# Kernel tuning notes

Measured on AMD Instinct MI355X. Metric: run time of the kernel, lower is better.

The kernel has to match this reference:

```python
import jax, jax.numpy as jnp
import numpy as np

B, D, NCLS = 65536, 784, 10

def sparse_layer(x, idx, w, b):
    # x: [B, D]; idx: [Dout, k] int; w: [Dout, k]; b: [Dout]
    # out[b, n] = sum_j x[b, idx[n, j]] * w[n, j] + b[n]
    g = x[:, idx]                      # [B, Dout, k] gather
    return jnp.einsum('bnk,nk->bn', g, w) + b

def setup_inputs() -> dict:
    key = jax.random.key(0)
    ks = jax.random.split(key, 12)
    def rn(k, shape, scale):
        return jax.random.normal(k, shape, dtype=jnp.float32) * scale
    return {
        'x': rn(ks[0], (B, D), 1.0),
        'idx1': jax.random.randint(ks[1], (D, 2), 0, D, dtype=jnp.int32),
        'w1': rn(ks[2], (D, 2), 0.5),
        'b1': rn(ks[3], (D,), 0.1),
        'idx2': jax.random.randint(ks[4], (D, 4), 0, D, dtype=jnp.int32),
        'w2': rn(ks[5], (D, 4), 0.4),
        'b2': rn(ks[6], (D,), 0.1),
        'idx3': jax.random.randint(ks[7], (D, 8), 0, D, dtype=jnp.int32),
        'w3': rn(ks[8], (D, 8), 0.3),
        'b3': rn(ks[9], (D,), 0.1),
        'fc_w': rn(ks[10], (NCLS, D), 0.05),
        'fc_b': rn(ks[11], (NCLS,), 0.05),
    }

def reference(x, idx1, w1, b1, idx2, w2, b2, idx3, w3, b3, fc_w, fc_b):
    h = jax.nn.gelu(sparse_layer(x, idx1, w1, b1), approximate=False)
    h = jax.nn.gelu(sparse_layer(h, idx2, w2, b2), approximate=False)
    h = jax.nn.gelu(sparse_layer(h, idx3, w3, b3), approximate=False)
    logits = h @ fc_w.T + fc_b          # [B, 10]
    return jax.nn.softmax(logits, axis=-1)
```

## Files before the change

kernel.cpp:

```cpp
#include <hip/hip_runtime.h>

#define D_     784
#define ROWS   8
#define NCLS   10
#define BLOCK  768
#define NB     (65536 / ROWS)
#define PL     (D_ * 4)
#define TAIL   (D_ - BLOCK)

__device__ __forceinline__ float gelu_f(float x) {
    float x2    = x * x;
    float inner = fmaf(0.044715f * x, x2, x);
    float e     = exp2f(2.3022082f * inner);
    float r     = __builtin_amdgcn_rcpf(e + 1.0f);
    return fmaf(-x, r, x);
}

__device__ __forceinline__ float4 gelu4(const float4& a) {
    return make_float4(gelu_f(a.x), gelu_f(a.y), gelu_f(a.z), gelu_f(a.w));
}

__device__ __forceinline__ void fma4(float4& a, const float4& h4, float wk) {
    a.x = fmaf(h4.x, wk, a.x);
    a.y = fmaf(h4.y, wk, a.y);
    a.z = fmaf(h4.z, wk, a.z);
    a.w = fmaf(h4.w, wk, a.w);
}

template <int K>
__device__ __forceinline__ void loadIdxW(const int* __restrict__ idx,
                                         const float* __restrict__ w,
                                         int n, int* jc, float* wc) {
    if constexpr (K == 2) {
        int2   j = *(const int2*)(idx + n * 2);
        float2 v = *(const float2*)(w + n * 2);
        jc[0] = j.x; jc[1] = j.y; wc[0] = v.x; wc[1] = v.y;
    } else if constexpr (K == 4) {
        int4   j = *(const int4*)(idx + n * 4);
        float4 v = *(const float4*)(w + n * 4);
        jc[0] = j.x; jc[1] = j.y; jc[2] = j.z; jc[3] = j.w;
        wc[0] = v.x; wc[1] = v.y; wc[2] = v.z; wc[3] = v.w;
    } else {
        int4   ja = *(const int4*)(idx + n * 8);
        int4   jb = *(const int4*)(idx + n * 8 + 4);
        float4 va = *(const float4*)(w + n * 8);
        float4 vb = *(const float4*)(w + n * 8 + 4);
        jc[0] = ja.x; jc[1] = ja.y; jc[2] = ja.z; jc[3] = ja.w;
        jc[4] = jb.x; jc[5] = jb.y; jc[6] = jb.z; jc[7] = jb.w;
        wc[0] = va.x; wc[1] = va.y; wc[2] = va.z; wc[3] = va.w;
        wc[4] = vb.x; wc[5] = vb.y; wc[6] = vb.z; wc[7] = vb.w;
    }
}

template <int K>
__device__ __forceinline__ void layer_one(const float* __restrict__ src,
                                          float* __restrict__ dst,
                                          const int* __restrict__ idx,
                                          const float* __restrict__ w,
                                          const float* __restrict__ bias,
                                          int n) {
    int   jc[K];
    float wc[K];
    loadIdxW<K>(idx, w, n, jc, wc);
    float  bc = bias[n];
    float4 lo = make_float4(bc, bc, bc, bc);
    float4 hi = lo;
#pragma unroll
    for (int k = 0; k < K; ++k) {
        const float* g = src + jc[k] * 4;
        float4 gl = *(const float4*)g;
        float4 gh = *(const float4*)(g + PL);
        fma4(lo, gl, wc[k]);
        fma4(hi, gh, wc[k]);
    }
    *(float4*)(dst + n * 4)      = gelu4(lo);
    *(float4*)(dst + n * 4 + PL) = gelu4(hi);
}

__global__ __launch_bounds__(BLOCK, 6)
void circnn_kernel(const float* __restrict__ x,
                   const int* __restrict__ idx1, const float* __restrict__ w1, const float* __restrict__ b1,
                   const int* __restrict__ idx2, const float* __restrict__ w2, const float* __restrict__ b2,
                   const int* __restrict__ idx3, const float* __restrict__ w3, const float* __restrict__ b3,
                   const float* __restrict__ fcw, const float* __restrict__ fcb,
                   float* __restrict__ out) {
    __shared__ __align__(16) float bufA[D_ * ROWS];
    __shared__ __align__(16) float bufB[D_ * ROWS];
    __shared__ float logits[ROWS * NCLS];

    const int tid  = threadIdx.x;
    const int row0 = blockIdx.x * ROWS;

    const float* xb = x + (size_t)row0 * D_;
    {
        int n = tid;
        float4 lo, hi;
        lo.x = xb[0 * D_ + n]; lo.y = xb[1 * D_ + n];
        lo.z = xb[2 * D_ + n]; lo.w = xb[3 * D_ + n];
        hi.x = xb[4 * D_ + n]; hi.y = xb[5 * D_ + n];
        hi.z = xb[6 * D_ + n]; hi.w = xb[7 * D_ + n];
        *(float4*)(bufA + n * 4)      = lo;
        *(float4*)(bufA + n * 4 + PL) = hi;
    }
    if (tid < TAIL) {
        int n = BLOCK + tid;
        float4 lo, hi;
        lo.x = xb[0 * D_ + n]; lo.y = xb[1 * D_ + n];
        lo.z = xb[2 * D_ + n]; lo.w = xb[3 * D_ + n];
        hi.x = xb[4 * D_ + n]; hi.y = xb[5 * D_ + n];
        hi.z = xb[6 * D_ + n]; hi.w = xb[7 * D_ + n];
        *(float4*)(bufA + n * 4)      = lo;
        *(float4*)(bufA + n * 4 + PL) = hi;
    }
    __syncthreads();

    layer_one<2>(bufA, bufB, idx1, w1, b1, tid);
    if (tid < TAIL) layer_one<2>(bufA, bufB, idx1, w1, b1, BLOCK + tid);
    __syncthreads();

    layer_one<4>(bufB, bufA, idx2, w2, b2, tid);
    if (tid < TAIL) layer_one<4>(bufB, bufA, idx2, w2, b2, BLOCK + tid);
    __syncthreads();

    layer_one<8>(bufA, bufB, idx3, w3, b3, tid);
    if (tid < TAIL) layer_one<8>(bufA, bufB, idx3, w3, b3, BLOCK + tid);
    __syncthreads();

    float4* part4 = (float4*)bufA;
    if (tid < 512) {
        const int p  = tid & 3;
        const int qq = (tid >> 2) & 1;
        const int jj = tid >> 3;
        float4 facc[NCLS];
#pragma unroll
        for (int c = 0; c < NCLS; ++c) facc[c] = make_float4(0.f, 0.f, 0.f, 0.f);
#pragma unroll 1
        for (int i = p; i < 13; i += 4) {
            int n = jj + (i << 6);
            if (n < D_) {
                float4 hv = *(const float4*)(bufB + qq * PL + n * 4);
#pragma unroll
                for (int c = 0; c < NCLS; ++c)
                    fma4(facc[c], hv, fcw[c * D_ + n]);
            }
        }
        float* f = (float*)facc;
#pragma unroll
        for (int t = 0; t < 4 * NCLS; ++t) {
            f[t] += __shfl_xor(f[t], 1);
            f[t] += __shfl_xor(f[t], 2);
        }
        if (p == 0) {
#pragma unroll
            for (int c = 0; c < NCLS; ++c)
                part4[(jj * 2 + qq) * NCLS + c] = facc[c];
        }
    }
    __syncthreads();

    if (tid < ROWS * NCLS) {
        int r = tid / NCLS, c = tid - r * NCLS;
        int qq = r >> 2, comp = r & 3;
        const float* pf = (const float*)part4;
        float s = fcb[c];
#pragma unroll 4
        for (int jj = 0; jj < 64; ++jj)
            s += pf[((jj * 2 + qq) * NCLS + c) * 4 + comp];
        logits[tid] = s;
    }
    __syncthreads();

    if (tid < ROWS * NCLS) {
        int r = tid / NCLS;
        const float* lg = logits + r * NCLS;
        float m = lg[0];
#pragma unroll
        for (int c = 1; c < NCLS; ++c) m = fmaxf(m, lg[c]);
        float s = 0.f;
#pragma unroll
        for (int c = 0; c < NCLS; ++c) s += __expf(lg[c] - m);
        out[(size_t)row0 * NCLS + tid] = __expf(logits[tid] - m) / s;
    }
}

extern "C" void kernel_launch(void* const* d_in, const int* in_sizes, int n_in,
                              void* d_out, int out_size, void* d_ws, size_t ws_size,
                              hipStream_t stream) {
    const float* x    = (const float*)d_in[0];
    const int*   idx1 = (const int*)d_in[1];
    const float* w1   = (const float*)d_in[2];
    const float* b1   = (const float*)d_in[3];
    const int*   idx2 = (const int*)d_in[4];
    const float* w2   = (const float*)d_in[5];
    const float* b2   = (const float*)d_in[6];
    const int*   idx3 = (const int*)d_in[7];
    const float* w3   = (const float*)d_in[8];
    const float* b3   = (const float*)d_in[9];
    const float* fcw  = (const float*)d_in[10];
    const float* fcb  = (const float*)d_in[11];
    float* out = (float*)d_out;

    circnn_kernel<<<dim3(NB), dim3(BLOCK), 0, stream>>>(
        x, idx1, w1, b1, idx2, w2, b2, idx3, w3, b3, fcw, fcb, out);
}
```

Measured before the change: 492.6 us.

## Halve rows per block to four with 512-thread blocks and padded partials

Each block now processes 4 batch rows instead of 8 with 512 threads, so each sparse-layer thread computes one float4 instead of two (lo/hi halves). Shared-memory buffers shrink and twice as many blocks launch, aiming for higher occupancy and less register pressure. The FC partial-sum layout is padded to 11 classes to reduce LDS bank conflicts. The tail pass now covers 272 columns instead of 16, so index/weight loads are amortized over fewer rows and more threads do a second pass.

```diff
diff --git a/kernel.cpp b/kernel.cpp
--- a/kernel.cpp
+++ b/kernel.cpp
@@ -1,11 +1,11 @@
 #include <hip/hip_runtime.h>
 
 #define D_     784
-#define ROWS   8
+#define ROWS   4
 #define NCLS   10
-#define BLOCK  768
+#define NCLSP  11
+#define BLOCK  512
 #define NB     (65536 / ROWS)
-#define PL     (D_ * 4)
 #define TAIL   (D_ - BLOCK)
 
 __device__ __forceinline__ float gelu_f(float x) {
@@ -63,21 +63,16 @@
     float wc[K];
     loadIdxW<K>(idx, w, n, jc, wc);
     float  bc = bias[n];
-    float4 lo = make_float4(bc, bc, bc, bc);
-    float4 hi = lo;
+    float4 a  = make_float4(bc, bc, bc, bc);
 #pragma unroll
     for (int k = 0; k < K; ++k) {
-        const float* g = src + jc[k] * 4;
-        float4 gl = *(const float4*)g;
-        float4 gh = *(const float4*)(g + PL);
-        fma4(lo, gl, wc[k]);
-        fma4(hi, gh, wc[k]);
+        float4 g = *(const float4*)(src + jc[k] * 4);
+        fma4(a, g, wc[k]);
     }
-    *(float4*)(dst + n * 4)      = gelu4(lo);
-    *(float4*)(dst + n * 4 + PL) = gelu4(hi);
+    *(float4*)(dst + n * 4) = gelu4(a);
 }
 
-__global__ __launch_bounds__(BLOCK, 6)
+__global__ __launch_bounds__(BLOCK)
 void circnn_kernel(const float* __restrict__ x,
                    const int* __restrict__ idx1, const float* __restrict__ w1, const float* __restrict__ b1,
                    const int* __restrict__ idx2, const float* __restrict__ w2, const float* __restrict__ b2,
@@ -94,23 +89,17 @@
     const float* xb = x + (size_t)row0 * D_;
     {
         int n = tid;
-        float4 lo, hi;
-        lo.x = xb[0 * D_ + n]; lo.y = xb[1 * D_ + n];
-        lo.z = xb[2 * D_ + n]; lo.w = xb[3 * D_ + n];
-        hi.x = xb[4 * D_ + n]; hi.y = xb[5 * D_ + n];
-        hi.z = xb[6 * D_ + n]; hi.w = xb[7 * D_ + n];
-        *(float4*)(bufA + n * 4)      = lo;
-        *(float4*)(bufA + n * 4 + PL) = hi;
+        float4 v;
+        v.x = xb[0 * D_ + n]; v.y = xb[1 * D_ + n];
+        v.z = xb[2 * D_ + n]; v.w = xb[3 * D_ + n];
+        *(float4*)(bufA + n * 4) = v;
     }
     if (tid < TAIL) {
         int n = BLOCK + tid;
-        float4 lo, hi;
-        lo.x = xb[0 * D_ + n]; lo.y = xb[1 * D_ + n];
-        lo.z = xb[2 * D_ + n]; lo.w = xb[3 * D_ + n];
-        hi.x = xb[4 * D_ + n]; hi.y = xb[5 * D_ + n];
-        hi.z = xb[6 * D_ + n]; hi.w = xb[7 * D_ + n];
-        *(float4*)(bufA + n * 4)      = lo;
-        *(float4*)(bufA + n * 4 + PL) = hi;
+        float4 v;
+        v.x = xb[0 * D_ + n]; v.y = xb[1 * D_ + n];
+        v.z = xb[2 * D_ + n]; v.w = xb[3 * D_ + n];
+        *(float4*)(bufA + n * 4) = v;
     }
     __syncthreads();
 
@@ -127,10 +116,9 @@
     __syncthreads();
 
     float4* part4 = (float4*)bufA;
-    if (tid < 512) {
+    if (tid < 256) {
         const int p  = tid & 3;
-        const int qq = (tid >> 2) & 1;
-        const int jj = tid >> 3;
+        const int jj = tid >> 2;
         float4 facc[NCLS];
 #pragma unroll
         for (int c = 0; c < NCLS; ++c) facc[c] = make_float4(0.f, 0.f, 0.f, 0.f);
@@ -138,34 +126,38 @@
         for (int i = p; i < 13; i += 4) {
             int n = jj + (i << 6);
             if (n < D_) {
-                float4 hv = *(const float4*)(bufB + qq * PL + n * 4);
+                float4 hv = *(const float4*)(bufB + n * 4);
 #pragma unroll
                 for (int c = 0; c < NCLS; ++c)
                     fma4(facc[c], hv, fcw[c * D_ + n]);
             }
         }
-        float* f = (float*)facc;
 #pragma unroll
-        for (int t = 0; t < 4 * NCLS; ++t) {
-            f[t] += __shfl_xor(f[t], 1);
-            f[t] += __shfl_xor(f[t], 2);
+        for (int c = 0; c < NCLS; ++c) {
+            facc[c].x += __shfl_xor(facc[c].x, 1);
+            facc[c].y += __shfl_xor(facc[c].y, 1);
+            facc[c].z += __shfl_xor(facc[c].z, 1);
+            facc[c].w += __shfl_xor(facc[c].w, 1);
+            facc[c].x += __shfl_xor(facc[c].x, 2);
+            facc[c].y += __shfl_xor(facc[c].y, 2);
+            facc[c].z += __shfl_xor(facc[c].z, 2);
+            facc[c].w += __shfl_xor(facc[c].w, 2);
         }
         if (p == 0) {
 #pragma unroll
             for (int c = 0; c < NCLS; ++c)
-                part4[(jj * 2 + qq) * NCLS + c] = facc[c];
+                part4[jj * NCLSP + c] = facc[c];
         }
     }
     __syncthreads();
 
     if (tid < ROWS * NCLS) {
         int r = tid / NCLS, c = tid - r * NCLS;
-        int qq = r >> 2, comp = r & 3;
         const float* pf = (const float*)part4;
         float s = fcb[c];
 #pragma unroll 4
         for (int jj = 0; jj < 64; ++jj)
-            s += pf[((jj * 2 + qq) * NCLS + c) * 4 + comp];
+            s += pf[(jj * NCLSP + c) * 4 + r];
         logits[tid] = s;
     }
     __syncthreads();
```

New measurement: 524.4 us. 6.4% more time.
